# Kernel optimization log

Measured on AMD Instinct MI355X. Metric: run time of the kernel, lower is better.

## Reference

```python
import jax, jax.numpy as jnp
import numpy as np

D = 128          # node_state_dim
N_NODES = 5000
WINDOW = 10
N_TOTAL = WINDOW * N_NODES
E = 131072       # structural (int) edges
T = 2            # message passing steps
HID = 1024


def setup_inputs() -> dict:
    key = jax.random.key(0)
    ks = jax.random.split(key, 20)
    ie = jax.random.randint(ks[0], (E, 3), 0, N_NODES, dtype=jnp.int32)
    int_edges = jnp.stack([ie[:, 0] % WINDOW, ie[:, 1], ie[:, 2]], axis=1)
    nodes = jax.random.randint(ks[1], (N_NODES,), 0, 10, dtype=jnp.int32)

    def init(k, shape, scale=0.05):
        return (jax.random.normal(k, shape, jnp.float32) * scale)

    params = dict(
        embed_table=init(ks[2], (10, D)),
        msg_W1=init(ks[3], (2 * D, HID)), msg_b1=jnp.zeros((HID,), jnp.float32),
        msg_W2=init(ks[4], (HID, D)), msg_b2=jnp.zeros((D,), jnp.float32),
        gru_int_W=init(ks[5], (D, 3 * D)), gru_int_U=init(ks[6], (D, 3 * D)),
        gru_int_b=jnp.zeros((2, 3 * D), jnp.float32),
        gru_temp_W=init(ks[7], (D, 3 * D)), gru_temp_U=init(ks[8], (D, 3 * D)),
        gru_temp_b=jnp.zeros((2, 3 * D), jnp.float32),
        ro_W1=init(ks[9], (D, HID)), ro_b1=jnp.zeros((HID,), jnp.float32),
        ro_W2=init(ks[10], (HID, 512)), ro_b2=jnp.zeros((512,), jnp.float32),
        ro_W3=init(ks[11], (512, 10)), ro_b3=jnp.zeros((10,), jnp.float32),
    )
    return {"int_edges": int_edges, "nodes": nodes, **params}


def _temp_edges():
    fwd_src = np.arange(0, N_TOTAL - N_NODES)
    fwd_dst = fwd_src + N_NODES
    bwd_src = np.arange(N_NODES, N_TOTAL)
    bwd_dst = bwd_src - N_NODES
    src = jnp.asarray(np.concatenate([fwd_src, bwd_src]), jnp.int32)
    dst = jnp.asarray(np.concatenate([fwd_dst, bwd_dst]), jnp.int32)
    return src, dst


def _gru(x, h, W, U, b):
    # Keras GRUCell, reset_after=True. x,h: [N,D]; W,U: [D,3D]; b: [2,3D]
    xg = x @ W + b[0]
    hg = h @ U + b[1]
    xz, xr, xh = jnp.split(xg, 3, axis=-1)
    hz, hr, hh = jnp.split(hg, 3, axis=-1)
    z = jax.nn.sigmoid(xz + hz)
    r = jax.nn.sigmoid(xr + hr)
    hcand = jnp.tanh(xh + r * hh)
    return z * h + (1.0 - z) * hcand


def _msg(x, W1, b1, W2, b2):
    # Dense(1024,relu) -> Dropout(inference: identity) -> Dense(D,relu)
    return jax.nn.relu(jax.nn.relu(x @ W1 + b1) @ W2 + b2)


def _seg_mean(x, idx, n):
    s = jax.ops.segment_sum(x, idx, num_segments=n)
    c = jax.ops.segment_sum(jnp.ones((x.shape[0],), x.dtype), idx, num_segments=n)
    return jnp.where(c[:, None] > 0, s / jnp.maximum(c, 1.0)[:, None], 0.0)


def reference(int_edges, nodes, embed_table, msg_W1, msg_b1, msg_W2, msg_b2,
              gru_int_W, gru_int_U, gru_int_b, gru_temp_W, gru_temp_U, gru_temp_b,
              ro_W1, ro_b1, ro_W2, ro_b2, ro_W3, ro_b3):
    node_idx = int_edges[:, 0] * N_NODES + int_edges[:, 1]        # [E]
    neigh_idx = int_edges[:, 0] * N_NODES + int_edges[:, 2]       # [E]
    t_src, t_dst = _temp_edges()

    h = embed_table[nodes]                                        # [n_nodes, D]
    h = jnp.repeat(h, WINDOW, axis=0)                             # [N_TOTAL, D]

    for _ in range(T):
        # structural edges
        m_in = jnp.concatenate([h[node_idx], h[neigh_idx]], axis=1)   # [E, 2D]
        m = _msg(m_in, msg_W1, msg_b1, msg_W2, msg_b2)                # [E, D]
        agg = _seg_mean(m, neigh_idx, N_TOTAL)                        # [N_TOTAL, D]
        h = _gru(agg, h, gru_int_W, gru_int_U, gru_int_b)
        # temporal edges
        tm_in = jnp.concatenate([h[t_src], h[t_dst]], axis=1)
        tm = _msg(tm_in, msg_W1, msg_b1, msg_W2, msg_b2)
        tagg = _seg_mean(tm, t_dst, N_TOTAL)
        h = _gru(tagg, h, gru_temp_W, gru_temp_U, gru_temp_b)

    # readout on first frame's nodes
    x = h[:N_NODES]
    x = jax.nn.relu(x @ ro_W1 + ro_b1)
    x = jax.nn.relu(x @ ro_W2 + ro_b2)
    return jax.nn.softmax(x @ ro_W3 + ro_b3, axis=-1)
```

## Files before the change

kernel.cpp:

```cpp
#include <hip/hip_runtime.h>
#include <math.h>

#define D 128
#define N_NODES 5000
#define WINDOW 10
#define N_TOTAL 50000
#define NE_INT 131072
#define NE_TMP 90000
#define NE_FWD (N_TOTAL - N_NODES)
#define HID 1024

typedef short bf16x8 __attribute__((ext_vector_type(8)));
typedef float f32x4 __attribute__((ext_vector_type(4)));

#define SA 264
#define SH 136
#define SK 136
#define SCAN_B 256

static __device__ __forceinline__ short f2bf(float f) {
    union { float f; unsigned u; } v; v.f = f;
    unsigned r = v.u + 0x7fffu + ((v.u >> 16) & 1u);
    return (short)(r >> 16);
}
static __device__ __forceinline__ float bf2f(short s) {
    union { unsigned u; float f; } v;
    v.u = ((unsigned)(unsigned short)s) << 16;
    return v.f;
}

__global__ void k_tcvt(const float* __restrict__ in, short* __restrict__ out, int K, int N) {
    int i = blockIdx.x * blockDim.x + threadIdx.x;
    if (i >= N * K) return;
    int n = i / K, k = i - n * K;
    out[i] = f2bf(in[(size_t)k * N + n]);
}

__global__ void k_init_h(const int* __restrict__ nodes, const float* __restrict__ embed,
                         float* __restrict__ h32, short* __restrict__ h16) {
    int i = blockIdx.x * blockDim.x + threadIdx.x;
    if (i >= N_TOTAL * D) return;
    int row = i >> 7;
    int c = i & 127;
    int n = nodes[row / WINDOW];
    float v = embed[n * D + c];
    h32[i] = v;
    h16[i] = f2bf(v);
}

__global__ void k_build_int_edges(const int* __restrict__ ie, int* __restrict__ src,
                                  int* __restrict__ dst, int* __restrict__ icnt) {
    int e = blockIdx.x * blockDim.x + threadIdx.x;
    if (e >= NE_INT) return;
    int t = ie[e * 3 + 0], a = ie[e * 3 + 1], b = ie[e * 3 + 2];
    int d = t * N_NODES + b;
    src[e] = t * N_NODES + a;
    dst[e] = d;
    atomicAdd(&icnt[d], 1);
}

__global__ void k_build_tmp_edges(int* __restrict__ src, int* __restrict__ dst) {
    int e = blockIdx.x * blockDim.x + threadIdx.x;
    if (e >= NE_TMP) return;
    int s, d;
    if (e < NE_FWD) { s = e; d = e + N_NODES; }
    else { int q = e - NE_FWD; s = q + N_NODES; d = q; }
    src[e] = s;
    dst[e] = d;
}

__global__ void k_scan_partial(const int* __restrict__ cnt, int* __restrict__ rowstart,
                               int* __restrict__ btot, int n) {
    __shared__ int s[SCAN_B];
    int tid = threadIdx.x;
    int i = blockIdx.x * SCAN_B + tid;
    int v = (i < n) ? cnt[i] : 0;
    s[tid] = v;
    __syncthreads();
    for (int off = 1; off < SCAN_B; off <<= 1) {
        int x = (tid >= off) ? s[tid - off] : 0;
        __syncthreads();
        s[tid] += x;
        __syncthreads();
    }
    if (i < n) rowstart[i] = s[tid] - v;
    if (tid == SCAN_B - 1) btot[blockIdx.x] = s[tid];
}

__global__ void k_scan_block(int* __restrict__ btot, int nb) {
    __shared__ int s[SCAN_B];
    int tid = threadIdx.x;
    int v = (tid < nb) ? btot[tid] : 0;
    s[tid] = v;
    __syncthreads();
    for (int off = 1; off < SCAN_B; off <<= 1) {
        int x = (tid >= off) ? s[tid - off] : 0;
        __syncthreads();
        s[tid] += x;
        __syncthreads();
    }
    if (tid < nb) btot[tid] = s[tid] - v;
}

__global__ void k_scan_add(int* __restrict__ rowstart, const int* __restrict__ btot,
                           int* __restrict__ cursor, int n, int total) {
    int i = blockIdx.x * blockDim.x + threadIdx.x;
    if (i < n) {
        int v = rowstart[i] + btot[i >> 8];
        rowstart[i] = v;
        cursor[i] = v;
    }
    if (i == 0) rowstart[n] = total;
}

__global__ void k_fill_csr(const int* __restrict__ dst, int nE, int* __restrict__ cursor,
                           int* __restrict__ eidx) {
    int e = blockIdx.x * blockDim.x + threadIdx.x;
    if (e >= nE) return;
    int p = atomicAdd(&cursor[dst[e]], 1);
    eidx[p] = e;
}

__global__ void __launch_bounds__(256, 3) k_h12_mfma(
    const short* __restrict__ h16, const short* __restrict__ W1cT,
    const float* __restrict__ b1, short* __restrict__ H12)
{
    __shared__ short As[128 * SK];
    int t = threadIdx.x;
    int nb = blockIdx.x * 128;
    int mb = blockIdx.y * 128;

    {
        int r = t >> 1, q = t & 1;
        int row = mb + r;
        int rc = (row < N_TOTAL) ? row : (N_TOTAL - 1);
        const uint4* ap = (const uint4*)(h16 + (size_t)rc * D);
        uint4* ao = (uint4*)(As + r * SK);
#pragma unroll
        for (int i = 0; i < 8; ++i) ao[q * 8 + i] = ap[q * 8 + i];
    }
    __syncthreads();

    int w = t >> 6, lane = t & 63, lm = lane & 15, lk = lane >> 4;

    f32x4 acc[2][8];
#pragma unroll
    for (int nt = 0; nt < 8; ++nt) {
        int col = nb + nt * 16 + lm;
        float bv = (col < HID) ? b1[col] : 0.f;
#pragma unroll
        for (int mt = 0; mt < 2; ++mt)
#pragma unroll
            for (int rg = 0; rg < 4; ++rg) acc[mt][nt][rg] = bv;
    }
#pragma unroll
    for (int kk = 0; kk < 4; ++kk) {
        int ko = kk * 32 + lk * 8;
        bf16x8 a0 = *(const bf16x8*)(As + (w * 32 + lm) * SK + ko);
        bf16x8 a1 = *(const bf16x8*)(As + (w * 32 + 16 + lm) * SK + ko);
#pragma unroll
        for (int nt = 0; nt < 8; ++nt) {
            bf16x8 bfr = *(const bf16x8*)(W1cT + (size_t)(nb + nt * 16 + lm) * D + ko);
            acc[0][nt] = __builtin_amdgcn_mfma_f32_16x16x32_bf16(a0, bfr, acc[0][nt], 0, 0, 0);
            acc[1][nt] = __builtin_amdgcn_mfma_f32_16x16x32_bf16(a1, bfr, acc[1][nt], 0, 0, 0);
        }
    }
#pragma unroll
    for (int mt = 0; mt < 2; ++mt)
#pragma unroll
        for (int rg = 0; rg < 4; ++rg) {
            int row = mb + w * 32 + mt * 16 + lk * 4 + rg;
            if (row >= N_TOTAL) continue;
            short* op = H12 + (size_t)row * 2048 + nb;
#pragma unroll
            for (int nt = 0; nt < 8; ++nt)
                op[nt * 16 + lm] = f2bf(acc[mt][nt][rg]);
        }
}

__global__ void __launch_bounds__(256, 3) k_msg2_mfma(
    const short* __restrict__ H12, const int* __restrict__ perm,
    const int* __restrict__ src, const int* __restrict__ dst, int nE,
    const short* __restrict__ W2T, const float* __restrict__ b2,
    short* __restrict__ m)
{
    __shared__ short S[2][64 * SH];
    __shared__ int es[64], ed[64];
    int t = threadIdx.x;
    int p0 = blockIdx.x * 64;

    if (t < 64) {
        int p = p0 + t;
        int pc = (p < nE) ? p : (nE - 1);
        int e = perm ? perm[pc] : pc;
        es[t] = src[e];
        ed[t] = dst[e];
    }
    __syncthreads();

    int w = t >> 6, lane = t & 63, lm = lane & 15, lk = lane >> 4;
    int r = t >> 2, q = t & 3;
    const short* p1 = H12 + (size_t)es[r] * 2048 + q * 32;
    const short* p2 = H12 + (size_t)ed[r] * 2048 + 1024 + q * 32;

    uint4 ra[4], rb[4];
#pragma unroll
    for (int i = 0; i < 4; ++i) {
        ra[i] = *(const uint4*)(p1 + i * 8);
        rb[i] = *(const uint4*)(p2 + i * 8);
    }

    f32x4 c2[2][4];
#pragma unroll
    for (int cs = 0; cs < 2; ++cs) {
        int out0 = w * 32 + cs * 16 + lk * 4;
#pragma unroll
        for (int et = 0; et < 4; ++et)
#pragma unroll
            for (int rg = 0; rg < 4; ++rg) c2[cs][et][rg] = b2[out0 + rg];
    }

    {
        uint4* sp = (uint4*)(S[0] + r * SH + q * 32);
#pragma unroll
        for (int i = 0; i < 4; ++i) {
            union { uint4 u; short s[8]; } pa, pb, po;
            pa.u = ra[i]; pb.u = rb[i];
#pragma unroll
            for (int j = 0; j < 8; ++j)
                po.s[j] = f2bf(fmaxf(bf2f(pa.s[j]) + bf2f(pb.s[j]), 0.f));
            sp[i] = po.u;
        }
    }

    for (int hc = 0; hc < 8; ++hc) {
        int cur = hc & 1;
        __syncthreads();
        if (hc < 7) {
            const short* q1 = p1 + (hc + 1) * 128;
            const short* q2 = p2 + (hc + 1) * 128;
#pragma unroll
            for (int i = 0; i < 4; ++i) {
                ra[i] = *(const uint4*)(q1 + i * 8);
                rb[i] = *(const uint4*)(q2 + i * 8);
            }
        }
#pragma unroll
        for (int kk = 0; kk < 4; ++kk) {
            int ko = kk * 32 + lk * 8;
            bf16x8 a0 = *(const bf16x8*)(W2T + (size_t)(w * 32 + lm) * 1024 + hc * 128 + ko);
            bf16x8 a1 = *(const bf16x8*)(W2T + (size_t)(w * 32 + 16 + lm) * 1024 + hc * 128 + ko);
            bf16x8 bf[4];
#pragma unroll
            for (int et = 0; et < 4; ++et)
                bf[et] = *(const bf16x8*)(S[cur] + (et * 16 + lm) * SH + ko);
#pragma unroll
            for (int et = 0; et < 4; ++et) {
                c2[0][et] = __builtin_amdgcn_mfma_f32_16x16x32_bf16(a0, bf[et], c2[0][et], 0, 0, 0);
                c2[1][et] = __builtin_amdgcn_mfma_f32_16x16x32_bf16(a1, bf[et], c2[1][et], 0, 0, 0);
            }
        }
        if (hc < 7) {
            uint4* sp = (uint4*)(S[cur ^ 1] + r * SH + q * 32);
#pragma unroll
            for (int i = 0; i < 4; ++i) {
                union { uint4 u; short s[8]; } pa, pb, po;
                pa.u = ra[i]; pb.u = rb[i];
#pragma unroll
                for (int j = 0; j < 8; ++j)
                    po.s[j] = f2bf(fmaxf(bf2f(pa.s[j]) + bf2f(pb.s[j]), 0.f));
                sp[i] = po.u;
            }
        }
    }

#pragma unroll
    for (int et = 0; et < 4; ++et) {
        int edge = et * 16 + lm;
        int p = p0 + edge;
        if (p >= nE) continue;
        short* rowp = m + (size_t)p * 128;
#pragma unroll
        for (int cs = 0; cs < 2; ++cs) {
            int out0 = w * 32 + cs * 16 + lk * 4;
            short4 sv;
            sv.x = f2bf(fmaxf(c2[cs][et][0], 0.f));
            sv.y = f2bf(fmaxf(c2[cs][et][1], 0.f));
            sv.z = f2bf(fmaxf(c2[cs][et][2], 0.f));
            sv.w = f2bf(fmaxf(c2[cs][et][3], 0.f));
            *(short4*)(rowp + out0) = sv;
        }
    }
}

__global__ void __launch_bounds__(256, 2) k_msg_mfma(
    const short* __restrict__ h16, const int* __restrict__ src, const int* __restrict__ dst,
    int nE, const short* __restrict__ W1T, const float* __restrict__ b1,
    const short* __restrict__ W2T, const float* __restrict__ b2,
    short* __restrict__ m)
{
    __shared__ short Ain[64 * SA];
    __shared__ short Hid[64 * SH];

    int t = threadIdx.x;
    int e0 = blockIdx.x * 64;

    {
        int r = t >> 2, q = t & 3;
        int e = e0 + r;
        int ec = (e < nE) ? e : (nE - 1);
        int s = src[ec], d = dst[ec];
        const uint4* ps = (const uint4*)(h16 + (size_t)s * D);
        const uint4* pd = (const uint4*)(h16 + (size_t)d * D);
        uint4* ao = (uint4*)(Ain + r * SA);
#pragma unroll
        for (int i = 0; i < 8; ++i) {
            int g = i * 4 + q;
            ao[g] = (i < 4) ? ps[g] : pd[g - 16];
        }
    }
    __syncthreads();

    int w = t >> 6, lane = t & 63;
    int lm = lane & 15, lk = lane >> 4;

    f32x4 c2[2][4];
#pragma unroll
    for (int cs = 0; cs < 2; ++cs) {
        int out0 = w * 32 + cs * 16 + lk * 4;
#pragma unroll
        for (int et = 0; et < 4; ++et)
#pragma unroll
            for (int rg = 0; rg < 4; ++rg) c2[cs][et][rg] = b2[out0 + rg];
    }

    for (int hc = 0; hc < 8; ++hc) {
        f32x4 c1[2][4];
#pragma unroll
        for (int cs = 0; cs < 2; ++cs) {
            int ch0 = hc * 128 + (2 * w + cs) * 16 + lk * 4;
#pragma unroll
            for (int et = 0; et < 4; ++et)
#pragma unroll
                for (int rg = 0; rg < 4; ++rg) c1[cs][et][rg] = b1[ch0 + rg];
        }
#pragma unroll
        for (int kk = 0; kk < 8; ++kk) {
            int ko = kk * 32 + lk * 8;
            bf16x8 a0 = *(const bf16x8*)(W1T + (size_t)(hc * 128 + (2 * w) * 16 + lm) * 256 + ko);
            bf16x8 a1 = *(const bf16x8*)(W1T + (size_t)(hc * 128 + (2 * w + 1) * 16 + lm) * 256 + ko);
            bf16x8 bf[4];
#pragma unroll
            for (int et = 0; et < 4; ++et)
                bf[et] = *(const bf16x8*)(Ain + (et * 16 + lm) * SA + ko);
#pragma unroll
            for (int et = 0; et < 4; ++et) {
                c1[0][et] = __builtin_amdgcn_mfma_f32_16x16x32_bf16(a0, bf[et], c1[0][et], 0, 0, 0);
                c1[1][et] = __builtin_amdgcn_mfma_f32_16x16x32_bf16(a1, bf[et], c1[1][et], 0, 0, 0);
            }
        }
        __syncthreads();
#pragma unroll
        for (int cs = 0; cs < 2; ++cs) {
            int ch_in = (2 * w + cs) * 16 + lk * 4;
#pragma unroll
            for (int et = 0; et < 4; ++et) {
                int edge = et * 16 + lm;
                short4 sv;
                sv.x = f2bf(fmaxf(c1[cs][et][0], 0.f));
                sv.y = f2bf(fmaxf(c1[cs][et][1], 0.f));
                sv.z = f2bf(fmaxf(c1[cs][et][2], 0.f));
                sv.w = f2bf(fmaxf(c1[cs][et][3], 0.f));
                *(short4*)(Hid + edge * SH + ch_in) = sv;
            }
        }
        __syncthreads();
#pragma unroll
        for (int kk = 0; kk < 4; ++kk) {
            int ko = kk * 32 + lk * 8;
            bf16x8 a0 = *(const bf16x8*)(W2T + (size_t)(w * 32 + lm) * 1024 + hc * 128 + ko);
            bf16x8 a1 = *(const bf16x8*)(W2T + (size_t)(w * 32 + 16 + lm) * 1024 + hc * 128 + ko);
            bf16x8 bf[4];
#pragma unroll
            for (int et = 0; et < 4; ++et)
                bf[et] = *(const bf16x8*)(Hid + (et * 16 + lm) * SH + ko);
#pragma unroll
            for (int et = 0; et < 4; ++et) {
                c2[0][et] = __builtin_amdgcn_mfma_f32_16x16x32_bf16(a0, bf[et], c2[0][et], 0, 0, 0);
                c2[1][et] = __builtin_amdgcn_mfma_f32_16x16x32_bf16(a1, bf[et], c2[1][et], 0, 0, 0);
            }
        }
    }

#pragma unroll
    for (int et = 0; et < 4; ++et) {
        int edge = et * 16 + lm;
        int e = e0 + edge;
        if (e >= nE) continue;
        short* rowp = m + (size_t)e * 128;
#pragma unroll
        for (int cs = 0; cs < 2; ++cs) {
            int out0 = w * 32 + cs * 16 + lk * 4;
            short4 sv;
            sv.x = f2bf(fmaxf(c2[cs][et][0], 0.f));
            sv.y = f2bf(fmaxf(c2[cs][et][1], 0.f));
            sv.z = f2bf(fmaxf(c2[cs][et][2], 0.f));
            sv.w = f2bf(fmaxf(c2[cs][et][3], 0.f));
            *(short4*)(rowp + out0) = sv;
        }
    }
}

__global__ void __launch_bounds__(256, 2) k_gru_mfma(
    const short* __restrict__ m, const int* __restrict__ rowstart,
    const int* __restrict__ midx, int mode,
    float* __restrict__ h32, short* __restrict__ h16,
    const short* __restrict__ WT, const short* __restrict__ UT,
    const float* __restrict__ b)
{
    __shared__ short Ax[64 * SK];
    __shared__ short Hx[64 * SK];
    int t = threadIdx.x;
    int r0 = blockIdx.x * 64;

    {
        int r = t >> 2, q = t & 3;
        int row = r0 + r;
        int rc = (row < N_TOTAL) ? row : (N_TOTAL - 1);
        const uint4* hp = (const uint4*)(h16 + (size_t)rc * D);
        uint4* hxo = (uint4*)(Hx + r * SK);
#pragma unroll
        for (int i = 0; i < 4; ++i) hxo[q * 4 + i] = hp[q * 4 + i];

        float acc[32];
#pragma unroll
        for (int i = 0; i < 32; ++i) acc[i] = 0.f;
        int deg = 0;
        if (row < N_TOTAL) {
            if (mode == 0) {
                int s0 = rowstart[row], s1 = rowstart[row + 1];
                deg = s1 - s0;
                for (int p = s0; p < s1; ++p) {
                    int e = midx ? midx[p] : p;
                    const uint4* mp = (const uint4*)(m + (size_t)e * 128 + q * 32);
#pragma unroll
                    for (int i = 0; i < 4; ++i) {
                        uint4 v = mp[i];
                        const short* sp = (const short*)&v;
#pragma unroll
                        for (int j = 0; j < 8; ++j) acc[i * 8 + j] += bf2f(sp[j]);
                    }
                }
            } else {
                if (row >= N_NODES) {
                    const uint4* mp = (const uint4*)(m + (size_t)(row - N_NODES) * 128 + q * 32);
                    ++deg;
#pragma unroll
                    for (int i = 0; i < 4; ++i) {
                        uint4 v = mp[i];
                        const short* sp = (const short*)&v;
#pragma unroll
                        for (int j = 0; j < 8; ++j) acc[i * 8 + j] += bf2f(sp[j]);
                    }
                }
                if (row < NE_FWD) {
                    const uint4* mp = (const uint4*)(m + (size_t)(NE_FWD + row) * 128 + q * 32);
                    ++deg;
#pragma unroll
                    for (int i = 0; i < 4; ++i) {
                        uint4 v = mp[i];
                        const short* sp = (const short*)&v;
#pragma unroll
                        for (int j = 0; j < 8; ++j) acc[i * 8 + j] += bf2f(sp[j]);
                    }
                }
            }
        }
        float inv = (deg > 0) ? 1.f / (float)deg : 0.f;
        uint4* axp = (uint4*)(Ax + r * SK + q * 32);
#pragma unroll
        for (int i = 0; i < 4; ++i) {
            union { uint4 u; short s[8]; } pk;
#pragma unroll
            for (int j = 0; j < 8; ++j) pk.s[j] = f2bf(acc[i * 8 + j] * inv);
            axp[i] = pk.u;
        }
    }
    __syncthreads();

    int w = t >> 6, lane = t & 63;
    int lm = lane & 15, lk = lane >> 4;

    for (int g = 0; g < 8; ++g) {
        int ch = g * 16 + lm;
        f32x4 cxz, cxr, cxh, chz, chr_, chh;
#pragma unroll
        for (int rg = 0; rg < 4; ++rg) {
            cxz[rg] = b[ch];        chz[rg] = b[384 + ch];
            cxr[rg] = b[128 + ch];  chr_[rg] = b[384 + 128 + ch];
            cxh[rg] = b[256 + ch];  chh[rg] = b[384 + 256 + ch];
        }
#pragma unroll
        for (int kk = 0; kk < 4; ++kk) {
            int ko = kk * 32 + lk * 8;
            bf16x8 ax = *(const bf16x8*)(Ax + (w * 16 + lm) * SK + ko);
            bf16x8 hx = *(const bf16x8*)(Hx + (w * 16 + lm) * SK + ko);
            bf16x8 bz = *(const bf16x8*)(WT + (size_t)(ch) * 128 + ko);
            bf16x8 br = *(const bf16x8*)(WT + (size_t)(128 + ch) * 128 + ko);
            bf16x8 bh = *(const bf16x8*)(WT + (size_t)(256 + ch) * 128 + ko);
            bf16x8 uz = *(const bf16x8*)(UT + (size_t)(ch) * 128 + ko);
            bf16x8 ur = *(const bf16x8*)(UT + (size_t)(128 + ch) * 128 + ko);
            bf16x8 uh = *(const bf16x8*)(UT + (size_t)(256 + ch) * 128 + ko);
            cxz = __builtin_amdgcn_mfma_f32_16x16x32_bf16(ax, bz, cxz, 0, 0, 0);
            cxr = __builtin_amdgcn_mfma_f32_16x16x32_bf16(ax, br, cxr, 0, 0, 0);
            cxh = __builtin_amdgcn_mfma_f32_16x16x32_bf16(ax, bh, cxh, 0, 0, 0);
            chz = __builtin_amdgcn_mfma_f32_16x16x32_bf16(hx, uz, chz, 0, 0, 0);
            chr_ = __builtin_amdgcn_mfma_f32_16x16x32_bf16(hx, ur, chr_, 0, 0, 0);
            chh = __builtin_amdgcn_mfma_f32_16x16x32_bf16(hx, uh, chh, 0, 0, 0);
        }
#pragma unroll
        for (int rg = 0; rg < 4; ++rg) {
            int row = r0 + w * 16 + lk * 4 + rg;
            if (row >= N_TOTAL) continue;
            float z = 1.f / (1.f + expf(-(cxz[rg] + chz[rg])));
            float r_ = 1.f / (1.f + expf(-(cxr[rg] + chr_[rg])));
            float hcv = tanhf(cxh[rg] + r_ * chh[rg]);
            size_t idx = (size_t)row * D + ch;
            float hold = h32[idx];
            float hnew = z * hold + (1.f - z) * hcv;
            h32[idx] = hnew;
            h16[idx] = f2bf(hnew);
        }
    }
}

__global__ void __launch_bounds__(256, 2) k_ro_mfma(
    const short* __restrict__ A16, const short* __restrict__ BT,
    const float* __restrict__ bias, float* __restrict__ C32, short* __restrict__ C16,
    int M, int N, int K)
{
    __shared__ short As[64 * SK];
    int t = threadIdx.x;
    int mb = blockIdx.y * 64;
    int nb = blockIdx.x * 128;
    int w = t >> 6, lane = t & 63;
    int lm = lane & 15, lk = lane >> 4;

    f32x4 acc[8];
#pragma unroll
    for (int nt = 0; nt < 8; ++nt) {
        float bv = bias[nb + nt * 16 + lm];
        acc[nt][0] = bv; acc[nt][1] = bv; acc[nt][2] = bv; acc[nt][3] = bv;
    }

    for (int kc = 0; kc < K; kc += 128) {
        __syncthreads();
        {
            int r = t >> 2, q = t & 3;
            int row = mb + r;
            int rc = (row < M) ? row : (M - 1);
            const uint4* ap = (const uint4*)(A16 + (size_t)rc * K + kc);
            uint4* ao = (uint4*)(As + r * SK);
#pragma unroll
            for (int i = 0; i < 4; ++i) ao[i * 4 + q] = ap[i * 4 + q];
        }
        __syncthreads();
#pragma unroll
        for (int kk = 0; kk < 4; ++kk) {
            int ko = kk * 32 + lk * 8;
            bf16x8 a = *(const bf16x8*)(As + (w * 16 + lm) * SK + ko);
#pragma unroll
            for (int nt = 0; nt < 8; ++nt) {
                bf16x8 bfr = *(const bf16x8*)(BT + (size_t)(nb + nt * 16 + lm) * K + kc + ko);
                acc[nt] = __builtin_amdgcn_mfma_f32_16x16x32_bf16(a, bfr, acc[nt], 0, 0, 0);
            }
        }
    }
#pragma unroll
    for (int nt = 0; nt < 8; ++nt) {
        int col = nb + nt * 16 + lm;
#pragma unroll
        for (int rg = 0; rg < 4; ++rg) {
            int row = mb + w * 16 + lk * 4 + rg;
            if (row >= M) continue;
            float v = fmaxf(acc[nt][rg], 0.f);
            if (C32) C32[(size_t)row * N + col] = v;
            if (C16) C16[(size_t)row * N + col] = f2bf(v);
        }
    }
}

__global__ void __launch_bounds__(64) k_logits_softmax(
    const float* __restrict__ r2, const float* __restrict__ W3,
    const float* __restrict__ b3, float* __restrict__ out)
{
    int row = blockIdx.x;
    int t = threadIdx.x;
    float p[10];
#pragma unroll
    for (int j = 0; j < 10; ++j) p[j] = 0.f;
    for (int k = t; k < 512; k += 64) {
        float v = r2[(size_t)row * 512 + k];
#pragma unroll
        for (int j = 0; j < 10; ++j) p[j] += v * W3[k * 10 + j];
    }
#pragma unroll
    for (int j = 0; j < 10; ++j) {
        float s = p[j];
        for (int off = 32; off > 0; off >>= 1) s += __shfl_down(s, off);
        p[j] = s;
    }
    if (t == 0) {
        float mx = -1e30f;
#pragma unroll
        for (int j = 0; j < 10; ++j) { p[j] += b3[j]; mx = fmaxf(mx, p[j]); }
        float sum = 0.f;
#pragma unroll
        for (int j = 0; j < 10; ++j) { p[j] = expf(p[j] - mx); sum += p[j]; }
        float inv = 1.f / sum;
#pragma unroll
        for (int j = 0; j < 10; ++j) out[(size_t)row * 10 + j] = p[j] * inv;
    }
}

extern "C" void kernel_launch(void* const* d_in, const int* in_sizes, int n_in,
                              void* d_out, int out_size, void* d_ws, size_t ws_size,
                              hipStream_t stream)
{
    const int*   ie    = (const int*)d_in[0];
    const int*   nodes = (const int*)d_in[1];
    const float* embed = (const float*)d_in[2];
    const float* mW1   = (const float*)d_in[3];
    const float* mb1   = (const float*)d_in[4];
    const float* mW2   = (const float*)d_in[5];
    const float* mb2   = (const float*)d_in[6];
    const float* giW   = (const float*)d_in[7];
    const float* giU   = (const float*)d_in[8];
    const float* gib   = (const float*)d_in[9];
    const float* gtW   = (const float*)d_in[10];
    const float* gtU   = (const float*)d_in[11];
    const float* gtb   = (const float*)d_in[12];
    const float* rW1   = (const float*)d_in[13];
    const float* rb1   = (const float*)d_in[14];
    const float* rW2   = (const float*)d_in[15];
    const float* rb2   = (const float*)d_in[16];
    const float* rW3   = (const float*)d_in[17];
    const float* rb3   = (const float*)d_in[18];
    float* out = (float*)d_out;

    char* ws = (char*)d_ws;
    size_t off = 0;
    auto alloc = [&](size_t bytes) {
        void* p = ws + off;
        off += (bytes + 255) & ~(size_t)255;
        return p;
    };
    float* h32   = (float*)alloc((size_t)N_TOTAL * D * 4);
    short* h16   = (short*)alloc((size_t)N_TOTAL * D * 2);
    short* m     = (short*)alloc((size_t)NE_INT * 128 * 2);
    int*   icnt  = (int*)alloc((size_t)N_TOTAL * 4);
    int*   rowst = (int*)alloc((size_t)(N_TOTAL + 1) * 4);
    int*   btot  = (int*)alloc(256 * 4);
    int*   curs  = (int*)alloc((size_t)N_TOTAL * 4);
    int*   eidx  = (int*)alloc((size_t)NE_INT * 4);
    int*   srcA  = (int*)alloc((size_t)NE_INT * 4);
    int*   dstA  = (int*)alloc((size_t)NE_INT * 4);
    int*   srcT  = (int*)alloc((size_t)NE_TMP * 4);
    int*   dstT  = (int*)alloc((size_t)NE_TMP * 4);
    short* mW1T  = (short*)alloc((size_t)HID * 256 * 2);
    short* mW2T  = (short*)alloc((size_t)D * HID * 2);
    short* giWT  = (short*)alloc((size_t)384 * D * 2);
    short* giUT  = (short*)alloc((size_t)384 * D * 2);
    short* gtWT  = (short*)alloc((size_t)384 * D * 2);
    short* gtUT  = (short*)alloc((size_t)384 * D * 2);
    short* rW1T  = (short*)alloc((size_t)HID * D * 2);
    short* rW2T  = (short*)alloc((size_t)512 * HID * 2);
    short* r1_16 = (short*)alloc((size_t)N_NODES * HID * 2);
    float* r2_32 = (float*)alloc((size_t)N_NODES * 512 * 4);
    short* W1cT  = (short*)alloc((size_t)2048 * D * 2);

    size_t h12_bytes = (size_t)N_TOTAL * 2048 * 2;
    bool useH12 = (off + h12_bytes <= ws_size);
    short* H12 = useH12 ? (short*)alloc(h12_bytes) : nullptr;

    auto tc = [&](const float* in, short* o, int K, int N) {
        k_tcvt<<<(N * K + 255) / 256, 256, 0, stream>>>(in, o, K, N);
    };
    tc(mW1, mW1T, 256, HID);
    tc(mW2, mW2T, HID, D);
    tc(giW, giWT, D, 384);
    tc(giU, giUT, D, 384);
    tc(gtW, gtWT, D, 384);
    tc(gtU, gtUT, D, 384);
    tc(rW1, rW1T, D, HID);
    tc(rW2, rW2T, HID, 512);
    if (useH12) {
        tc(mW1, W1cT, D, HID);
        tc(mW1 + (size_t)D * HID, W1cT + (size_t)HID * D, D, HID);
    }

    hipMemsetAsync(icnt, 0, (size_t)N_TOTAL * 4, stream);
    k_init_h<<<(N_TOTAL * D + 255) / 256, 256, 0, stream>>>(nodes, embed, h32, h16);
    k_build_int_edges<<<(NE_INT + 255) / 256, 256, 0, stream>>>(ie, srcA, dstA, icnt);
    k_build_tmp_edges<<<(NE_TMP + 255) / 256, 256, 0, stream>>>(srcT, dstT);
    int nb = (N_TOTAL + SCAN_B - 1) / SCAN_B;
    k_scan_partial<<<nb, SCAN_B, 0, stream>>>(icnt, rowst, btot, N_TOTAL);
    k_scan_block<<<1, SCAN_B, 0, stream>>>(btot, nb);
    k_scan_add<<<nb, SCAN_B, 0, stream>>>(rowst, btot, curs, N_TOTAL, NE_INT);
    k_fill_csr<<<(NE_INT + 255) / 256, 256, 0, stream>>>(dstA, NE_INT, curs, eidx);

    int gmsgA = (NE_INT + 63) / 64;
    int gmsgT = (NE_TMP + 63) / 64;
    int ggru = (N_TOTAL + 63) / 64;
    dim3 gh12(2048 / 128, (N_TOTAL + 127) / 128);
    for (int it = 0; it < 2; ++it) {
        if (useH12) {
            k_h12_mfma<<<gh12, 256, 0, stream>>>(h16, W1cT, mb1, H12);
            k_msg2_mfma<<<gmsgA, 256, 0, stream>>>(H12, eidx, srcA, dstA, NE_INT, mW2T, mb2, m);
            k_gru_mfma<<<ggru, 256, 0, stream>>>(m, rowst, (const int*)nullptr, 0, h32, h16, giWT, giUT, gib);

            k_h12_mfma<<<gh12, 256, 0, stream>>>(h16, W1cT, mb1, H12);
            k_msg2_mfma<<<gmsgT, 256, 0, stream>>>(H12, (const int*)nullptr, srcT, dstT, NE_TMP, mW2T, mb2, m);
            k_gru_mfma<<<ggru, 256, 0, stream>>>(m, rowst, (const int*)nullptr, 1, h32, h16, gtWT, gtUT, gtb);
        } else {
            k_msg_mfma<<<gmsgA, 256, 0, stream>>>(h16, srcA, dstA, NE_INT, mW1T, mb1, mW2T, mb2, m);
            k_gru_mfma<<<ggru, 256, 0, stream>>>(m, rowst, eidx, 0, h32, h16, giWT, giUT, gib);

            k_msg_mfma<<<gmsgT, 256, 0, stream>>>(h16, srcT, dstT, NE_TMP, mW1T, mb1, mW2T, mb2, m);
            k_gru_mfma<<<ggru, 256, 0, stream>>>(m, rowst, eidx, 1, h32, h16, gtWT, gtUT, gtb);
        }
    }

    dim3 g1(HID / 128, (N_NODES + 63) / 64);
    k_ro_mfma<<<g1, 256, 0, stream>>>(h16, rW1T, rb1, (float*)nullptr, r1_16, N_NODES, HID, D);
    dim3 g2(512 / 128, (N_NODES + 63) / 64);
    k_ro_mfma<<<g2, 256, 0, stream>>>(r1_16, rW2T, rb2, r2_32, (short*)nullptr, N_NODES, 512, HID);
    k_logits_softmax<<<N_NODES, 64, 0, stream>>>(r2_32, rW3, rb3, out);
}
```

Measured before the change: 1.297 ms.

## Slice structural message pass per window frame to keep H12 cache-resident

Structural edges never cross window frames, so the precomputed first-layer projection (H12) is now built and consumed one frame at a time. A 5000-row buffer replaces the 50000-row one, so the per-edge gathers should hit in cache instead of streaming a very large buffer from HBM. The readout scratch buffers are aliased onto the freed space. The temporal pass drops the H12 path and goes back to the fused per-edge MLP kernel, which redoes the first-layer work per edge. The structural pass also needs ten times as many launches per iteration.

```diff
diff --git a/kernel.cpp b/kernel.cpp
--- a/kernel.cpp
+++ b/kernel.cpp
@@ -123,7 +123,7 @@
 
 __global__ void __launch_bounds__(256, 3) k_h12_mfma(
     const short* __restrict__ h16, const short* __restrict__ W1cT,
-    const float* __restrict__ b1, short* __restrict__ H12)
+    const float* __restrict__ b1, short* __restrict__ H12s, int row0, int nrows)
 {
     __shared__ short As[128 * SK];
     int t = threadIdx.x;
@@ -132,9 +132,9 @@
 
     {
         int r = t >> 1, q = t & 1;
-        int row = mb + r;
-        int rc = (row < N_TOTAL) ? row : (N_TOTAL - 1);
-        const uint4* ap = (const uint4*)(h16 + (size_t)rc * D);
+        int lr = mb + r;
+        int rc = (lr < nrows) ? lr : (nrows - 1);
+        const uint4* ap = (const uint4*)(h16 + (size_t)(row0 + rc) * D);
         uint4* ao = (uint4*)(As + r * SK);
 #pragma unroll
         for (int i = 0; i < 8; ++i) ao[q * 8 + i] = ap[q * 8 + i];
@@ -169,99 +169,66 @@
     for (int mt = 0; mt < 2; ++mt)
 #pragma unroll
         for (int rg = 0; rg < 4; ++rg) {
-            int row = mb + w * 32 + mt * 16 + lk * 4 + rg;
-            if (row >= N_TOTAL) continue;
-            short* op = H12 + (size_t)row * 2048 + nb;
+            int lr = mb + w * 32 + mt * 16 + lk * 4 + rg;
+            if (lr >= nrows) continue;
+            short* op = H12s + (size_t)lr * 2048 + nb;
 #pragma unroll
             for (int nt = 0; nt < 8; ++nt)
                 op[nt * 16 + lm] = f2bf(acc[mt][nt][rg]);
         }
 }
 
-__global__ void __launch_bounds__(256, 3) k_msg2_mfma(
-    const short* __restrict__ H12, const int* __restrict__ perm,
-    const int* __restrict__ src, const int* __restrict__ dst, int nE,
+__global__ void __launch_bounds__(256, 3) k_msg2_int(
+    const short* __restrict__ H12s, const int* __restrict__ eidx,
+    const int* __restrict__ src, const int* __restrict__ dst,
+    const int* __restrict__ rowstart, int slice,
     const short* __restrict__ W2T, const float* __restrict__ b2,
     short* __restrict__ m)
 {
     __shared__ short S[2][64 * SH];
     __shared__ int es[64], ed[64];
     int t = threadIdx.x;
-    int p0 = blockIdx.x * 64;
-
-    if (t < 64) {
-        int p = p0 + t;
-        int pc = (p < nE) ? p : (nE - 1);
-        int e = perm ? perm[pc] : pc;
-        es[t] = src[e];
-        ed[t] = dst[e];
-    }
-    __syncthreads();
+    int base = slice * N_NODES;
+    int s_lo = rowstart[base];
+    int s_hi = rowstart[base + N_NODES];
+    int ngroups = (s_hi - s_lo + 63) >> 6;
 
     int w = t >> 6, lane = t & 63, lm = lane & 15, lk = lane >> 4;
     int r = t >> 2, q = t & 3;
-    const short* p1 = H12 + (size_t)es[r] * 2048 + q * 32;
-    const short* p2 = H12 + (size_t)ed[r] * 2048 + 1024 + q * 32;
-
-    uint4 ra[4], rb[4];
-#pragma unroll
-    for (int i = 0; i < 4; ++i) {
-        ra[i] = *(const uint4*)(p1 + i * 8);
-        rb[i] = *(const uint4*)(p2 + i * 8);
-    }
-
-    f32x4 c2[2][4];
-#pragma unroll
-    for (int cs = 0; cs < 2; ++cs) {
-        int out0 = w * 32 + cs * 16 + lk * 4;
-#pragma unroll
-        for (int et = 0; et < 4; ++et)
-#pragma unroll
-            for (int rg = 0; rg < 4; ++rg) c2[cs][et][rg] = b2[out0 + rg];
-    }
-
-    {
-        uint4* sp = (uint4*)(S[0] + r * SH + q * 32);
+
+    for (int g = blockIdx.x; g < ngroups; g += gridDim.x) {
+        int p0 = s_lo + g * 64;
+        __syncthreads();
+        if (t < 64) {
+            int p = p0 + t;
+            int pc = (p < s_hi) ? p : (s_hi - 1);
+            int e = eidx[pc];
+            es[t] = src[e] - base;
+            ed[t] = dst[e] - base;
+        }
+        __syncthreads();
+
+        const short* p1 = H12s + (size_t)es[r] * 2048 + q * 32;
+        const short* p2 = H12s + (size_t)ed[r] * 2048 + 1024 + q * 32;
+
+        uint4 ra[4], rb[4];
 #pragma unroll
         for (int i = 0; i < 4; ++i) {
-            union { uint4 u; short s[8]; } pa, pb, po;
-            pa.u = ra[i]; pb.u = rb[i];
-#pragma unroll
-            for (int j = 0; j < 8; ++j)
-                po.s[j] = f2bf(fmaxf(bf2f(pa.s[j]) + bf2f(pb.s[j]), 0.f));
-            sp[i] = po.u;
-        }
-    }
-
-    for (int hc = 0; hc < 8; ++hc) {
-        int cur = hc & 1;
-        __syncthreads();
-        if (hc < 7) {
-            const short* q1 = p1 + (hc + 1) * 128;
-            const short* q2 = p2 + (hc + 1) * 128;
-#pragma unroll
-            for (int i = 0; i < 4; ++i) {
-                ra[i] = *(const uint4*)(q1 + i * 8);
-                rb[i] = *(const uint4*)(q2 + i * 8);
-            }
-        }
-#pragma unroll
-        for (int kk = 0; kk < 4; ++kk) {
-            int ko = kk * 32 + lk * 8;
-            bf16x8 a0 = *(const bf16x8*)(W2T + (size_t)(w * 32 + lm) * 1024 + hc * 128 + ko);
-            bf16x8 a1 = *(const bf16x8*)(W2T + (size_t)(w * 32 + 16 + lm) * 1024 + hc * 128 + ko);
-            bf16x8 bf[4];
+            ra[i] = *(const uint4*)(p1 + i * 8);
+            rb[i] = *(const uint4*)(p2 + i * 8);
+        }
+
+        f32x4 c2[2][4];
+#pragma unroll
+        for (int cs = 0; cs < 2; ++cs) {
+            int out0 = w * 32 + cs * 16 + lk * 4;
 #pragma unroll
             for (int et = 0; et < 4; ++et)
-                bf[et] = *(const bf16x8*)(S[cur] + (et * 16 + lm) * SH + ko);
-#pragma unroll
-            for (int et = 0; et < 4; ++et) {
-                c2[0][et] = __builtin_amdgcn_mfma_f32_16x16x32_bf16(a0, bf[et], c2[0][et], 0, 0, 0);
-                c2[1][et] = __builtin_amdgcn_mfma_f32_16x16x32_bf16(a1, bf[et], c2[1][et], 0, 0, 0);
-            }
-        }
-        if (hc < 7) {
-            uint4* sp = (uint4*)(S[cur ^ 1] + r * SH + q * 32);
+#pragma unroll
+                for (int rg = 0; rg < 4; ++rg) c2[cs][et][rg] = b2[out0 + rg];
+        }
+        {
+            uint4* sp = (uint4*)(S[0] + r * SH + q * 32);
 #pragma unroll
             for (int i = 0; i < 4; ++i) {
                 union { uint4 u; short s[8]; } pa, pb, po;
@@ -272,23 +239,64 @@
                 sp[i] = po.u;
             }
         }
-    }
-
-#pragma unroll
-    for (int et = 0; et < 4; ++et) {
-        int edge = et * 16 + lm;
-        int p = p0 + edge;
-        if (p >= nE) continue;
-        short* rowp = m + (size_t)p * 128;
-#pragma unroll
-        for (int cs = 0; cs < 2; ++cs) {
-            int out0 = w * 32 + cs * 16 + lk * 4;
-            short4 sv;
-            sv.x = f2bf(fmaxf(c2[cs][et][0], 0.f));
-            sv.y = f2bf(fmaxf(c2[cs][et][1], 0.f));
-            sv.z = f2bf(fmaxf(c2[cs][et][2], 0.f));
-            sv.w = f2bf(fmaxf(c2[cs][et][3], 0.f));
-            *(short4*)(rowp + out0) = sv;
+
+        for (int hc = 0; hc < 8; ++hc) {
+            int cur = hc & 1;
+            __syncthreads();
+            if (hc < 7) {
+                const short* q1 = p1 + (hc + 1) * 128;
+                const short* q2 = p2 + (hc + 1) * 128;
+#pragma unroll
+                for (int i = 0; i < 4; ++i) {
+                    ra[i] = *(const uint4*)(q1 + i * 8);
+                    rb[i] = *(const uint4*)(q2 + i * 8);
+                }
+            }
+#pragma unroll
+            for (int kk = 0; kk < 4; ++kk) {
+                int ko = kk * 32 + lk * 8;
+                bf16x8 a0 = *(const bf16x8*)(W2T + (size_t)(w * 32 + lm) * 1024 + hc * 128 + ko);
+                bf16x8 a1 = *(const bf16x8*)(W2T + (size_t)(w * 32 + 16 + lm) * 1024 + hc * 128 + ko);
+                bf16x8 bf[4];
+#pragma unroll
+                for (int et = 0; et < 4; ++et)
+                    bf[et] = *(const bf16x8*)(S[cur] + (et * 16 + lm) * SH + ko);
+#pragma unroll
+                for (int et = 0; et < 4; ++et) {
+                    c2[0][et] = __builtin_amdgcn_mfma_f32_16x16x32_bf16(a0, bf[et], c2[0][et], 0, 0, 0);
+                    c2[1][et] = __builtin_amdgcn_mfma_f32_16x16x32_bf16(a1, bf[et], c2[1][et], 0, 0, 0);
+                }
+            }
+            if (hc < 7) {
+                uint4* sp = (uint4*)(S[cur ^ 1] + r * SH + q * 32);
+#pragma unroll
+                for (int i = 0; i < 4; ++i) {
+                    union { uint4 u; short s[8]; } pa, pb, po;
+                    pa.u = ra[i]; pb.u = rb[i];
+#pragma unroll
+                    for (int j = 0; j < 8; ++j)
+                        po.s[j] = f2bf(fmaxf(bf2f(pa.s[j]) + bf2f(pb.s[j]), 0.f));
+                    sp[i] = po.u;
+                }
+            }
+        }
+
+#pragma unroll
+        for (int et = 0; et < 4; ++et) {
+            int edge = et * 16 + lm;
+            int p = p0 + edge;
+            if (p >= s_hi) continue;
+            short* rowp = m + (size_t)p * 128;
+#pragma unroll
+            for (int cs = 0; cs < 2; ++cs) {
+                int out0 = w * 32 + cs * 16 + lk * 4;
+                short4 sv;
+                sv.x = f2bf(fmaxf(c2[cs][et][0], 0.f));
+                sv.y = f2bf(fmaxf(c2[cs][et][1], 0.f));
+                sv.z = f2bf(fmaxf(c2[cs][et][2], 0.f));
+                sv.w = f2bf(fmaxf(c2[cs][et][3], 0.f));
+                *(short4*)(rowp + out0) = sv;
+            }
         }
     }
 }
@@ -675,13 +683,11 @@
     short* gtUT  = (short*)alloc((size_t)384 * D * 2);
     short* rW1T  = (short*)alloc((size_t)HID * D * 2);
     short* rW2T  = (short*)alloc((size_t)512 * HID * 2);
-    short* r1_16 = (short*)alloc((size_t)N_NODES * HID * 2);
-    float* r2_32 = (float*)alloc((size_t)N_NODES * 512 * 4);
     short* W1cT  = (short*)alloc((size_t)2048 * D * 2);
 
-    size_t h12_bytes = (size_t)N_TOTAL * 2048 * 2;
-    bool useH12 = (off + h12_bytes <= ws_size);
-    short* H12 = useH12 ? (short*)alloc(h12_bytes) : nullptr;
+    short* H12s  = (short*)alloc((size_t)N_NODES * 2048 * 2);
+    short* r1_16 = H12s;
+    float* r2_32 = (float*)(H12s + (size_t)N_NODES * 1024);
 
     auto tc = [&](const float* in, short* o, int K, int N) {
         k_tcvt<<<(N * K + 255) / 256, 256, 0, stream>>>(in, o, K, N);
@@ -694,10 +700,8 @@
     tc(gtU, gtUT, D, 384);
     tc(rW1, rW1T, D, HID);
     tc(rW2, rW2T, HID, 512);
-    if (useH12) {
-        tc(mW1, W1cT, D, HID);
-        tc(mW1 + (size_t)D * HID, W1cT + (size_t)HID * D, D, HID);
-    }
+    tc(mW1, W1cT, D, HID);
+    tc(mW1 + (size_t)D * HID, W1cT + (size_t)HID * D, D, HID);
 
     hipMemsetAsync(icnt, 0, (size_t)N_TOTAL * 4, stream);
     k_init_h<<<(N_TOTAL * D + 255) / 256, 256, 0, stream>>>(nodes, embed, h32, h16);
@@ -709,26 +713,18 @@
     k_scan_add<<<nb, SCAN_B, 0, stream>>>(rowst, btot, curs, N_TOTAL, NE_INT);
     k_fill_csr<<<(NE_INT + 255) / 256, 256, 0, stream>>>(dstA, NE_INT, curs, eidx);
 
-    int gmsgA = (NE_INT + 63) / 64;
     int gmsgT = (NE_TMP + 63) / 64;
     int ggru = (N_TOTAL + 63) / 64;
-    dim3 gh12(2048 / 128, (N_TOTAL + 127) / 128);
+    dim3 gh12(2048 / 128, (N_NODES + 127) / 128);
     for (int it = 0; it < 2; ++it) {
-        if (useH12) {
-            k_h12_mfma<<<gh12, 256, 0, stream>>>(h16, W1cT, mb1, H12);
-            k_msg2_mfma<<<gmsgA, 256, 0, stream>>>(H12, eidx, srcA, dstA, NE_INT, mW2T, mb2, m);
-            k_gru_mfma<<<ggru, 256, 0, stream>>>(m, rowst, (const int*)nullptr, 0, h32, h16, giWT, giUT, gib);
-
-            k_h12_mfma<<<gh12, 256, 0, stream>>>(h16, W1cT, mb1, H12);
-            k_msg2_mfma<<<gmsgT, 256, 0, stream>>>(H12, (const int*)nullptr, srcT, dstT, NE_TMP, mW2T, mb2, m);
-            k_gru_mfma<<<ggru, 256, 0, stream>>>(m, rowst, (const int*)nullptr, 1, h32, h16, gtWT, gtUT, gtb);
-        } else {
-            k_msg_mfma<<<gmsgA, 256, 0, stream>>>(h16, srcA, dstA, NE_INT, mW1T, mb1, mW2T, mb2, m);
-            k_gru_mfma<<<ggru, 256, 0, stream>>>(m, rowst, eidx, 0, h32, h16, giWT, giUT, gib);
-
-            k_msg_mfma<<<gmsgT, 256, 0, stream>>>(h16, srcT, dstT, NE_TMP, mW1T, mb1, mW2T, mb2, m);
-            k_gru_mfma<<<ggru, 256, 0, stream>>>(m, rowst, eidx, 1, h32, h16, gtWT, gtUT, gtb);
-        }
+        for (int sl = 0; sl < WINDOW; ++sl) {
+            k_h12_mfma<<<gh12, 256, 0, stream>>>(h16, W1cT, mb1, H12s, sl * N_NODES, N_NODES);
+            k_msg2_int<<<256, 256, 0, stream>>>(H12s, eidx, srcA, dstA, rowst, sl, mW2T, mb2, m);
+        }
+        k_gru_mfma<<<ggru, 256, 0, stream>>>(m, rowst, (const int*)nullptr, 0, h32, h16, giWT, giUT, gib);
+
+        k_msg_mfma<<<gmsgT, 256, 0, stream>>>(h16, srcT, dstT, NE_TMP, mW1T, mb1, mW2T, mb2, m);
+        k_gru_mfma<<<ggru, 256, 0, stream>>>(m, rowst, (const int*)nullptr, 1, h32, h16, gtWT, gtUT, gtb);
     }
 
     dim3 g1(HID / 128, (N_NODES + 63) / 64);
```

New measurement: 1.820 ms. 1.4x slower.
